# Kernel optimization log

Measured on AMD Instinct MI355X. Metric: run time of the kernel, lower is better.

Reference implementation:

```python
import jax, jax.numpy as jnp
import numpy as np

B, D, H = 4096, 32, 1024  # batch, in_out_dim, hidden width


def setup_inputs() -> dict:
    key = jax.random.key(0)
    ks = jax.random.split(key, 10)

    def lin_w(k, shape, fan_in):
        bound = 1.0 / np.sqrt(fan_in)
        return jax.random.uniform(k, shape, jnp.float32, -bound, bound)

    return {
        "t": jax.random.uniform(ks[0], (1,), jnp.float32),
        "z": jax.random.normal(ks[1], (B, D), jnp.float32),
        "W0": lin_w(ks[2], (H, D + 1), D + 1),
        "b0": lin_w(ks[3], (H,), D + 1),
        "W1": lin_w(ks[4], (H, H), H),
        "b1": lin_w(ks[5], (H,), H),
        "W2": lin_w(ks[6], (H, H), H),
        "b2": lin_w(ks[7], (H,), H),
        "W3": lin_w(ks[8], (D, H), H),
        "b3": lin_w(ks[9], (D,), H),
    }


def _mlp(v, params):
    # Linear -> Tanh chain, final Linear (torch convention y = x @ W.T + b)
    for W, b in params[:-1]:
        v = jnp.tanh(v @ W.T + b)
    W, b = params[-1]
    return v @ W.T + b


def reference(t, z, W0, b0, W1, b1, W2, b2, W3, b3):
    bsz, d = z.shape
    tt = jnp.broadcast_to(t.reshape(-1), (bsz,))  # check_t: repeat scalar t
    params = [(W0, b0), (W1, b1), (W2, b2), (W3, b3)]

    def f(zz):  # [B, D] -> [B, D]
        v = jnp.concatenate([zz, tt[:, None]], axis=1)  # [B, D+1]
        return _mlp(v, params)

    out = f(z)

    # Exact Jacobian trace via d forward-mode JVPs (replaces the per-dim
    # autograd.grad loop in trace_df_dz with a single vmapped JVP batch).
    eye = jnp.eye(d, dtype=z.dtype)

    def jvp_i(e):
        return jax.jvp(f, (z,), (jnp.broadcast_to(e, z.shape),))[1]  # [B, D]

    tang = jax.vmap(jvp_i)(eye)            # [D, B, D]
    trace = jnp.einsum("ibi->b", tang)     # sum_i df_i/dz_i per sample
    divv = -trace
    return out, divv[:, None]
```

## Files before the change

kernel.cpp:

```cpp
#include <hip/hip_runtime.h>
#include <hip/hip_bf16.h>
#include <stdint.h>


using bf  = __hip_bfloat16;
using bf2 = __hip_bfloat162;
typedef __attribute__((ext_vector_type(8))) short bf16x8;
typedef __attribute__((ext_vector_type(4))) float f32x4;

__device__ __forceinline__ float b2f(bf x)    { return __bfloat162float(x); }
__device__ __forceinline__ bf    f2b(float x) { return __float2bfloat16(x); }

__device__ __forceinline__ void gld16(const void* g, void* l) {
  __builtin_amdgcn_global_load_lds((const __attribute__((address_space(1))) void*)g,
                                   (__attribute__((address_space(3))) void*)l,
                                   16, 0, 0);
}

__device__ __forceinline__ void conv_body(int blk, const float* __restrict__ src,
                                          bf* __restrict__ dst, int n4) {
  const int i = blk * 256 + threadIdx.x;
  if (i >= n4) return;
  float4 v = ((const float4*)src)[i];
  bf2* d = (bf2*)(dst + (size_t)i * 4);
  d[0] = __float22bfloat162_rn(make_float2(v.x, v.y));
  d[1] = __float22bfloat162_rn(make_float2(v.z, v.w));
}

__device__ __forceinline__ void w0t_body(int blk, const float* __restrict__ W0,
                                         bf* __restrict__ W0T) {
  const int idx = blk * 256 + threadIdx.x;
  const int i = idx >> 10, q = idx & 1023;
  W0T[idx] = f2b(W0[q * 33 + i]);
}

__global__ __launch_bounds__(256) void prep_k(const float* __restrict__ z,
                                              const float* __restrict__ tin,
                                              const float* __restrict__ W0,
                                              const float* __restrict__ b0,
                                              const float* __restrict__ W1,
                                              const float* __restrict__ W2,
                                              const float* __restrict__ W3,
                                              bf* __restrict__ h0,
                                              bf* __restrict__ W0T,
                                              bf* __restrict__ W1b,
                                              bf* __restrict__ W2b,
                                              bf* __restrict__ W3b,
                                              float* __restrict__ out2) {
  __shared__ float zs[32 * 33];
  const int f = blockIdx.x, t = threadIdx.x;
  if (f < 128) {
    const int s0 = f * 32;
    for (int j = t; j < 1024; j += 256) {
      const int s = j >> 5, k = j & 31;
      zs[s * 33 + k] = z[(size_t)(s0 + s) * 32 + k];
    }
    if (t < 32) zs[t * 33 + 32] = tin[0];
    __syncthreads();
#pragma unroll 1
    for (int rep = 0; rep < 4; ++rep) {
      const int hh = rep * 256 + t;
      const float* wr = W0 + (size_t)hh * 33;
      float wv[33];
#pragma unroll
      for (int k = 0; k < 33; ++k) wv[k] = wr[k];
      const float bv = b0[hh];
#pragma unroll 1
      for (int s = 0; s < 32; ++s) {
        float acc = bv;
#pragma unroll
        for (int k = 0; k < 33; ++k) acc += wv[k] * zs[s * 33 + k];
        h0[(size_t)(s0 + s) * 1024 + hh] = f2b(tanhf(acc));
      }
    }
  } else if (f < 1152) {
    conv_body(f - 128, W1, W1b, 262144);
  } else if (f < 2176) {
    conv_body(f - 1152, W2, W2b, 262144);
  } else if (f < 2208) {
    conv_body(f - 2176, W3, W3b, 8192);
  } else if (f < 2336) {
    w0t_body(f - 2208, W0, W0T);
  } else {
#pragma unroll
    for (int u = 0; u < 16; ++u) out2[u * 256 + t] = 0.f;
  }
}

__device__ __forceinline__ void gemm_core(bf* As, bf* Bs,
                                          const bf* __restrict__ A,
                                          const bf* __restrict__ B,
                                          size_t m0, size_t n0,
                                          f32x4 (&acc)[8][4]) {
  constexpr int K = 1024;
  const int t = threadIdx.x, l = t & 63, w = t >> 6;
  const int wm = w >> 1, wn = w & 1;
  const int r15 = l & 15, q4 = l >> 4, sw = r15 & 7;

  const int lrow = l >> 3;
  const int lseg = (l & 7) ^ lrow;
  const bf* asrc[8]; bf* alds[8];
  const bf* bsrc[4]; bf* blds[4];
#pragma unroll
  for (int u = 0; u < 8; ++u) {
    const int row = w * 64 + u * 8 + lrow;
    asrc[u] = A + (m0 + row) * K + lseg * 8;
    alds[u] = As + (size_t)(w * 64 + u * 8) * 64;
  }
#pragma unroll
  for (int u = 0; u < 4; ++u) {
    const int row = w * 32 + u * 8 + lrow;
    bsrc[u] = B + (n0 + row) * K + lseg * 8;
    blds[u] = Bs + (size_t)(w * 32 + u * 8) * 64;
  }

#pragma unroll 1
  for (int k0 = 0; k0 < K; k0 += 64) {
#pragma unroll
    for (int u = 0; u < 8; ++u) gld16(asrc[u] + k0, alds[u]);
#pragma unroll
    for (int u = 0; u < 4; ++u) gld16(bsrc[u] + k0, blds[u]);
    __syncthreads();
#pragma unroll
    for (int kk = 0; kk < 2; ++kk) {
      const int sa = (kk * 4 + q4) ^ sw;
      bf16x8 af[8], bfr[4];
#pragma unroll
      for (int i = 0; i < 8; ++i)
        af[i] = *(const bf16x8*)(As + (wm * 128 + i * 16 + r15) * 64 + sa * 8);
#pragma unroll
      for (int j = 0; j < 4; ++j)
        bfr[j] = *(const bf16x8*)(Bs + (wn * 64 + j * 16 + r15) * 64 + sa * 8);
#pragma unroll
      for (int mi = 0; mi < 8; ++mi)
#pragma unroll
        for (int ni = 0; ni < 4; ++ni)
          acc[mi][ni] = __builtin_amdgcn_mfma_f32_16x16x32_bf16(af[mi], bfr[ni], acc[mi][ni], 0, 0, 0);
    }
    __syncthreads();
  }
}

__global__ __launch_bounds__(256, 2) void gemm_fwd(const bf* __restrict__ A,
                                                   const bf* __restrict__ W,
                                                   const float* __restrict__ bias,
                                                   bf* __restrict__ H) {
  constexpr int N = 1024;
  __shared__ __align__(16) bf As[256 * 64];
  __shared__ __align__(16) bf Bs[128 * 64];
  const int t = threadIdx.x, l = t & 63, w = t >> 6;
  const int wm = w >> 1, wn = w & 1;
  const int f = blockIdx.x;
  const int n_t = (f >> 3) & 7, m_t = (f & 7) + 8 * (f >> 6);
  const size_t m0 = (size_t)m_t * 256, n0 = (size_t)n_t * 128;
  const int r15 = l & 15, q4 = l >> 4;
  f32x4 acc[8][4] = {};
  gemm_core(As, Bs, A, W, m0, n0, acc);
#pragma unroll
  for (int ni = 0; ni < 4; ++ni) {
    const int n = (int)n0 + wn * 64 + ni * 16 + r15;
    const float bv = bias[n];
#pragma unroll
    for (int mi = 0; mi < 8; ++mi)
#pragma unroll
      for (int r = 0; r < 4; ++r) {
        const size_t m = m0 + wm * 128 + mi * 16 + q4 * 4 + r;
        H[m * N + n] = f2b(tanhf(acc[mi][ni][r] + bv));
      }
  }
}

__global__ __launch_bounds__(256) void fwd3_k(const bf* __restrict__ h2,
                                              const bf* __restrict__ W3b,
                                              const float* __restrict__ b3,
                                              float* __restrict__ out) {
  __shared__ __align__(16) bf hs[8 * 1024];
  const int t = threadIdx.x;
  const size_t bb = (size_t)blockIdx.x * 8;
  const uint4* src = (const uint4*)(h2 + bb * 1024);
  uint4* dv = (uint4*)hs;
#pragma unroll
  for (int j = 0; j < 4; ++j) dv[j * 256 + t] = src[j * 256 + t];
  __syncthreads();
  const int i = t & 31, bl = t >> 5;
  const bf2* hr = (const bf2*)(hs + bl * 1024);
  const bf2* wr = (const bf2*)(W3b + (size_t)i * 1024);
  float s = 0.f;
#pragma unroll 8
  for (int k2 = 0; k2 < 512; ++k2) {
    float2 a = __bfloat1622float2(hr[k2]);
    float2 c = __bfloat1622float2(wr[k2]);
    s += a.x * c.x + a.y * c.y;
  }
  out[(bb + bl) * 32 + i] = s + b3[i];
}

__global__ __launch_bounds__(256) void t0_k(const bf* __restrict__ h0c,
                                            const bf* __restrict__ W0T,
                                            bf* __restrict__ T0) {
  const int idx = blockIdx.x * 256 + threadIdx.x;
  const int m = idx >> 6, seg = idx & 63;
  const int b = m >> 5, i = m & 31;
  const bf2* hp = (const bf2*)(h0c + (size_t)b * 1024 + seg * 16);
  const bf2* wp = (const bf2*)(W0T + (size_t)i * 1024 + seg * 16);
  bf2* dp = (bf2*)(T0 + (size_t)m * 1024 + seg * 16);
#pragma unroll
  for (int u = 0; u < 8; ++u) {
    float2 h = __bfloat1622float2(hp[u]);
    float2 w = __bfloat1622float2(wp[u]);
    float2 r;
    r.x = (1.f - h.x * h.x) * w.x;
    r.y = (1.f - h.y * h.y) * w.y;
    dp[u] = __float22bfloat162_rn(r);
  }
}

__device__ __forceinline__ void gemm8_core(bf* lds,
                                           const bf* __restrict__ A,
                                           const bf* __restrict__ B,
                                           size_t m0, size_t n0,
                                           f32x4 (&acc)[8][4]) {
  constexpr int K = 1024;
  const int t = threadIdx.x, l = t & 63, w = t >> 6;
  const int wm = w >> 2, wn = w & 3;
  const int r15 = l & 15, q4 = l >> 4;
  const int lrow = l >> 3, lseg = (l & 7) ^ lrow;
  const int w8 = w * 8;

  bf* As0 = lds;          bf* As1 = lds + 16384;
  bf* Bs0 = lds + 32768;  bf* Bs1 = lds + 49152;

  const bf* Ag = A + (m0 + (size_t)(w8 + lrow)) * K + lseg * 8;
  const bf* Bg = B + (n0 + (size_t)(w8 + lrow)) * K + lseg * 8;

  const int sa0 = q4 ^ (r15 & 7);
  const int aoff = (wm * 128 + r15) * 64;
  const int boff = (wn * 64 + r15) * 64;

  bf16x8 bfr[4][2];
  bf16x8 af[2][2];

  auto ldB = [&](const bf* Bsp) {
#pragma unroll
    for (int ni = 0; ni < 4; ++ni) {
      bfr[ni][0] = *(const bf16x8*)(Bsp + boff + ni * 1024 + sa0 * 8);
      bfr[ni][1] = *(const bf16x8*)(Bsp + boff + ni * 1024 + (sa0 ^ 4) * 8);
    }
  };
  auto ldA = [&](const bf* Asp, int q) {
#pragma unroll
    for (int s = 0; s < 2; ++s) {
      af[s][0] = *(const bf16x8*)(Asp + aoff + (2 * q + s) * 1024 + sa0 * 8);
      af[s][1] = *(const bf16x8*)(Asp + aoff + (2 * q + s) * 1024 + (sa0 ^ 4) * 8);
    }
  };
  auto stA = [&](bf* dst, int kt, int h) {
    gld16(Ag + (size_t)(h * 128) * K + kt * 64,      dst + (h * 128 + w8) * 64);
    gld16(Ag + (size_t)(h * 128 + 64) * K + kt * 64, dst + (h * 128 + 64 + w8) * 64);
  };
  auto stB = [&](bf* dst, int kt, int h) {
    gld16(Bg + (size_t)(h * 128) * K + kt * 64,      dst + (h * 128 + w8) * 64);
    gld16(Bg + (size_t)(h * 128 + 64) * K + kt * 64, dst + (h * 128 + 64 + w8) * 64);
  };
  auto mmq = [&](int q) {
    __builtin_amdgcn_s_barrier();
    asm volatile("s_waitcnt lgkmcnt(0)");
    __builtin_amdgcn_s_setprio(1);
#pragma unroll
    for (int kk = 0; kk < 2; ++kk)
#pragma unroll
      for (int s = 0; s < 2; ++s)
#pragma unroll
        for (int ni = 0; ni < 4; ++ni)
          acc[2 * q + s][ni] = __builtin_amdgcn_mfma_f32_16x16x32_bf16(
              af[s][kk], bfr[ni][kk], acc[2 * q + s][ni], 0, 0, 0);
    __builtin_amdgcn_s_setprio(0);
    __builtin_amdgcn_s_barrier();
  };

  stA(As0, 0, 0); stA(As0, 0, 1);
  stB(Bs0, 0, 0); stB(Bs0, 0, 1);
  stB(Bs1, 1, 0); stB(Bs1, 1, 1);
  asm volatile("s_waitcnt vmcnt(4)" ::: "memory");
  __builtin_amdgcn_s_barrier();

#pragma unroll 1
  for (int j = 0; j < 8; ++j) {
    const int o = 2 * j + 1, e2 = (2 * j + 2) & 15, o2 = (2 * j + 3) & 15;
    ldB(Bs0); ldA(As0, 0); stA(As1, o, 0);            mmq(0);
    ldA(As0, 1);           stA(As1, o, 1);            mmq(1);
    ldA(As0, 2);           stB(Bs0, e2, 0);           mmq(2);
    ldA(As0, 3);           stB(Bs0, e2, 1);
    asm volatile("s_waitcnt vmcnt(4)" ::: "memory");  mmq(3);
    ldB(Bs1); ldA(As1, 0); stA(As0, e2, 0);           mmq(0);
    ldA(As1, 1);           stA(As0, e2, 1);           mmq(1);
    ldA(As1, 2);           stB(Bs1, o2, 0);           mmq(2);
    ldA(As1, 3);           stB(Bs1, o2, 1);
    asm volatile("s_waitcnt vmcnt(4)" ::: "memory");  mmq(3);
  }
  asm volatile("s_waitcnt vmcnt(0)" ::: "memory");
}

__global__ __launch_bounds__(512, 2) void gemm8_jvp1(const bf* __restrict__ T0,
                                                     const bf* __restrict__ W1b,
                                                     const bf* __restrict__ h1c,
                                                     bf* __restrict__ T1) {
  __shared__ __align__(16) bf lds[65536];
  const int f = blockIdx.x;
  const size_t m0 = (size_t)(f >> 2) * 256, n0 = (size_t)(f & 3) * 256;
  f32x4 acc[8][4] = {};
  gemm8_core(lds, T0, W1b, m0, n0, acc);
  const int t = threadIdx.x, l = t & 63, w = t >> 6;
  const int wm = w >> 2, wn = w & 3;
  const int r15 = l & 15, q4 = l >> 4;
  const int bbase = (int)((m0 + wm * 128) >> 5);
#pragma unroll
  for (int ni = 0; ni < 4; ++ni) {
    const int n = (int)n0 + wn * 64 + ni * 16 + r15;
    float a1v[4];
#pragma unroll
    for (int s = 0; s < 4; ++s) {
      const float hv = b2f(h1c[(size_t)(bbase + s) * 1024 + n]);
      a1v[s] = 1.f - hv * hv;
    }
#pragma unroll
    for (int mi = 0; mi < 8; ++mi)
#pragma unroll
      for (int r = 0; r < 4; ++r) {
        const size_t m = m0 + wm * 128 + mi * 16 + q4 * 4 + r;
        T1[m * 1024 + n] = f2b(a1v[mi >> 1] * acc[mi][ni][r]);
      }
  }
}

__global__ __launch_bounds__(512, 2) void gemm8_jvp2(const bf* __restrict__ T1,
                                                     const bf* __restrict__ W2b,
                                                     const bf* __restrict__ W3b,
                                                     const bf* __restrict__ h2c,
                                                     float* __restrict__ out2c) {
  __shared__ __align__(16) bf lds[65536];
  const int f = blockIdx.x;
  const size_t m0 = (size_t)(f >> 2) * 256, n0 = (size_t)(f & 3) * 256;
  f32x4 acc[8][4] = {};
  gemm8_core(lds, T1, W2b, m0, n0, acc);
  const int t = threadIdx.x, l = t & 63, w = t >> 6;
  const int wm = w >> 2, wn = w & 3;
  const int r15 = l & 15, q4 = l >> 4;
  const int bbase = (int)((m0 + wm * 128) >> 5);
  float part[4] = {0.f, 0.f, 0.f, 0.f};
#pragma unroll
  for (int ni = 0; ni < 4; ++ni) {
    const int n = (int)n0 + wn * 64 + ni * 16 + r15;
    float a2v[4];
#pragma unroll
    for (int s = 0; s < 4; ++s) {
      const float hv = b2f(h2c[(size_t)(bbase + s) * 1024 + n]);
      a2v[s] = 1.f - hv * hv;
    }
#pragma unroll
    for (int mi = 0; mi < 8; ++mi) {
      const int isel = mi >> 1;
#pragma unroll
      for (int r = 0; r < 4; ++r) {
        const int mm = wm * 128 + mi * 16 + q4 * 4 + r;
        part[isel] += b2f(W3b[(size_t)(mm & 31) * 1024 + n]) * a2v[isel] * acc[mi][ni][r];
      }
    }
  }
#pragma unroll
  for (int off = 32; off > 0; off >>= 1) {
#pragma unroll
    for (int s = 0; s < 4; ++s) part[s] += __shfl_down(part[s], off);
  }
  if (l == 0) {
#pragma unroll
    for (int s = 0; s < 4; ++s) atomicAdd(out2c + bbase + s, -part[s]);
  }
}

extern "C" void kernel_launch(void* const* d_in, const int* in_sizes, int n_in,
                              void* d_out, int out_size, void* d_ws, size_t ws_size,
                              hipStream_t stream) {
  const float* tin = (const float*)d_in[0];
  const float* z   = (const float*)d_in[1];
  const float* W0  = (const float*)d_in[2];
  const float* b0  = (const float*)d_in[3];
  const float* W1  = (const float*)d_in[4];
  const float* b1  = (const float*)d_in[5];
  const float* W2  = (const float*)d_in[6];
  const float* b2  = (const float*)d_in[7];
  const float* W3  = (const float*)d_in[8];
  const float* b3  = (const float*)d_in[9];
  float* out = (float*)d_out;
  float* out2 = out + 131072;
  (void)in_sizes; (void)n_in; (void)out_size;

  char* ws = (char*)d_ws;
  size_t off = 0;
  auto take = [&](size_t bytes) {
    char* p = ws + off;
    off = (off + bytes + 255) & ~(size_t)255;
    return p;
  };
  bf* h0   = (bf*)take((size_t)4096 * 1024 * 2);
  bf* h1   = (bf*)take((size_t)4096 * 1024 * 2);
  bf* h2   = (bf*)take((size_t)4096 * 1024 * 2);
  bf* W0T  = (bf*)take((size_t)32 * 1024 * 2);
  bf* W1b  = (bf*)take((size_t)1024 * 1024 * 2);
  bf* W2b  = (bf*)take((size_t)1024 * 1024 * 2);
  bf* W3b  = (bf*)take((size_t)32 * 1024 * 2);
  const size_t avail = (ws_size > off) ? (ws_size - off) : 0;
  int NB = 4096;
  while (NB > 256 && 2 * (size_t)NB * 65536 > avail) NB >>= 1;
  bf* T0 = (bf*)take((size_t)NB * 65536);
  bf* T1 = (bf*)take((size_t)NB * 65536);

  prep_k<<<dim3(2337), dim3(256), 0, stream>>>(z, tin, W0, b0, W1, W2, W3,
                                               h0, W0T, W1b, W2b, W3b, out2);
  gemm_fwd<<<dim3(128), dim3(256), 0, stream>>>(h0, W1b, b1, h1);
  gemm_fwd<<<dim3(128), dim3(256), 0, stream>>>(h1, W2b, b2, h2);
  fwd3_k<<<dim3(512), dim3(256), 0, stream>>>(h2, W3b, b3, out);
  for (int cb = 0; cb < 4096; cb += NB) {
    t0_k<<<dim3(NB * 8), dim3(256), 0, stream>>>(h0 + (size_t)cb * 1024, W0T, T0);
    gemm8_jvp1<<<dim3(NB / 2), dim3(512), 0, stream>>>(
        T0, W1b, h1 + (size_t)cb * 1024, T1);
    gemm8_jvp2<<<dim3(NB / 2), dim3(512), 0, stream>>>(
        T1, W2b, W3b, h2 + (size_t)cb * 1024, out2 + cb);
  }
}
```

Measured before the change: 824.2 us.

## Triple-buffer A tiles in GEMM core and swizzle workgroups across XCDs

Measured after the change: 871.0 us. +5.7%, slower.

```diff
diff --git a/kernel.cpp b/kernel.cpp
--- a/kernel.cpp
+++ b/kernel.cpp
@@ -227,9 +227,6 @@
   const int lrow = l >> 3, lseg = (l & 7) ^ lrow;
   const int w8 = w * 8;
 
-  bf* As0 = lds;          bf* As1 = lds + 16384;
-  bf* Bs0 = lds + 32768;  bf* Bs1 = lds + 49152;
-
   const bf* Ag = A + (m0 + (size_t)(w8 + lrow)) * K + lseg * 8;
   const bf* Bg = B + (n0 + (size_t)(w8 + lrow)) * K + lseg * 8;
 
@@ -278,35 +275,41 @@
     __builtin_amdgcn_s_barrier();
   };
 
-  stA(As0, 0, 0); stA(As0, 0, 1);
-  stB(Bs0, 0, 0); stB(Bs0, 0, 1);
-  stB(Bs1, 1, 0); stB(Bs1, 1, 1);
-  asm volatile("s_waitcnt vmcnt(4)" ::: "memory");
+  bf* A0 = lds;          bf* A1 = lds + 16384;  bf* A2 = lds + 32768;
+  bf* B0 = lds + 49152;  bf* B1 = lds + 65536;
+
+  stA(A0, 0, 0); stA(A0, 0, 1); stB(B0, 0, 0); stB(B0, 0, 1);
+  stA(A1, 1, 0); stA(A1, 1, 1); stB(B1, 1, 0); stB(B1, 1, 1);
+  asm volatile("s_waitcnt vmcnt(8)" ::: "memory");
   __builtin_amdgcn_s_barrier();
 
+  bf* Rd = A0; bf* Nx = A1; bf* Wr = A2;
+  bf* Brd = B0; bf* Bot = B1;
 #pragma unroll 1
-  for (int j = 0; j < 8; ++j) {
-    const int o = 2 * j + 1, e2 = (2 * j + 2) & 15, o2 = (2 * j + 3) & 15;
-    ldB(Bs0); ldA(As0, 0); stA(As1, o, 0);            mmq(0);
-    ldA(As0, 1);           stA(As1, o, 1);            mmq(1);
-    ldA(As0, 2);           stB(Bs0, e2, 0);           mmq(2);
-    ldA(As0, 3);           stB(Bs0, e2, 1);
-    asm volatile("s_waitcnt vmcnt(4)" ::: "memory");  mmq(3);
-    ldB(Bs1); ldA(As1, 0); stA(As0, e2, 0);           mmq(0);
-    ldA(As1, 1);           stA(As0, e2, 1);           mmq(1);
-    ldA(As1, 2);           stB(Bs1, o2, 0);           mmq(2);
-    ldA(As1, 3);           stB(Bs1, o2, 1);
-    asm volatile("s_waitcnt vmcnt(4)" ::: "memory");  mmq(3);
+  for (int tt = 0; tt < 16; ++tt) {
+    const int k2 = (tt + 2) & 15;
+    ldB(Brd); ldA(Rd, 0); stA(Wr, k2, 0);   mmq(0);
+    ldA(Rd, 1);           stA(Wr, k2, 1);   mmq(1);
+    ldA(Rd, 2);           stB(Brd, k2, 0);  mmq(2);
+    ldA(Rd, 3);           stB(Brd, k2, 1);
+    asm volatile("s_waitcnt vmcnt(8)" ::: "memory");
+    mmq(3);
+    bf* tmp = Rd; Rd = Nx; Nx = Wr; Wr = tmp;
+    tmp = Brd; Brd = Bot; Bot = tmp;
   }
   asm volatile("s_waitcnt vmcnt(0)" ::: "memory");
+}
+
+__device__ __forceinline__ int xcd_swz(int f0, int nwg) {
+  return (f0 & 7) * (nwg >> 3) + (f0 >> 3);
 }
 
 __global__ __launch_bounds__(512, 2) void gemm8_jvp1(const bf* __restrict__ T0,
                                                      const bf* __restrict__ W1b,
                                                      const bf* __restrict__ h1c,
                                                      bf* __restrict__ T1) {
-  __shared__ __align__(16) bf lds[65536];
-  const int f = blockIdx.x;
+  __shared__ __align__(16) bf lds[81920];
+  const int f = xcd_swz(blockIdx.x, gridDim.x);
   const size_t m0 = (size_t)(f >> 2) * 256, n0 = (size_t)(f & 3) * 256;
   f32x4 acc[8][4] = {};
   gemm8_core(lds, T0, W1b, m0, n0, acc);
@@ -338,8 +341,8 @@
                                                      const bf* __restrict__ W3b,
                                                      const bf* __restrict__ h2c,
                                                      float* __restrict__ out2c) {
-  __shared__ __align__(16) bf lds[65536];
-  const int f = blockIdx.x;
+  __shared__ __align__(16) bf lds[81920];
+  const int f = xcd_swz(blockIdx.x, gridDim.x);
   const size_t m0 = (size_t)(f >> 2) * 256, n0 = (size_t)(f & 3) * 256;
   f32x4 acc[8][4] = {};
   gemm8_core(lds, T1, W2b, m0, n0, acc);
```
